# Performance work log

Hardware: AMD Instinct MI355X
Metric: run time of the kernel (lower is better)

The kernel has to match this reference:

```python
import jax, jax.numpy as jnp
import numpy as np

N_NODES = 25000
N_EDGES = 400000
N_GRAPHS = 100
D_IN = 16
D = 32          # node_dim
K = 11          # spectral coefficients = edge_dim
NOUT1 = 30
NOUT2 = 2
L = 2           # n_interactions
D_OUT = 32


def setup_inputs() -> dict:
    key = jax.random.key(0)
    ks = jax.random.split(key, 24)
    s = 0.1
    inp = {
        'x': jax.random.normal(ks[0], (N_NODES, D_IN), jnp.float32),
        'edge_attr': jax.random.uniform(ks[1], (N_EDGES, K), jnp.float32),
        'edge_index': jax.random.randint(ks[2], (2, N_EDGES), 0, N_NODES),
        'batch': jnp.sort(jax.random.randint(ks[3], (N_NODES,), 0, N_GRAPHS)),
        # embedding
        'emb_w': jax.random.normal(ks[4], (D_IN, D)) * s,
        'emb_b': jnp.zeros((D,)),
        # per-interaction params, stacked on leading L axis
        'init_w': jax.random.normal(ks[5], (L, D, D)) * s,             # initial_dense (no bias)
        'e1_w': jax.random.normal(ks[6], (L, K, 2 * K)) * s,
        'e2_w': jax.random.normal(ks[7], (L, K, 2 * K)) * s,
        'e3_w': jax.random.normal(ks[8], (L, K, 2 * K)) * s,
        'e4_w': jax.random.normal(ks[9], (L, 4 * K, K)) * s,
        'conv_w': jax.random.normal(ks[10], (L, K, D, NOUT1)) * s,     # SpectConv weight (selfconn=False)
        'conv_b': jnp.zeros((L, NOUT1)),
        'att_v': jax.random.normal(ks[11], (L, D, 1)) * s,
        'skip1_w': jax.random.normal(ks[12], (L, D, NOUT2)) * s,
        'skip1_b': jnp.full((L, NOUT2), 0.01),
        'skip2_w': jax.random.normal(ks[13], (L, D, NOUT2)) * s,
        'skip2_b': jnp.full((L, NOUT2), 0.01),
        'out_w': jax.random.normal(ks[14], (L, NOUT1 + NOUT2, D)) * s,
        'out_b': jnp.full((L, D), 0.01),
        # encoder output head
        'final_w': jax.random.normal(ks[15], (D, D_OUT)) * s,
        'final_b': jnp.zeros((D_OUT,)),
    }
    return inp


def _segment_softmax(raw, dst, n):
    m = jax.ops.segment_max(raw, dst, num_segments=n)
    m = jnp.where(jnp.isfinite(m), m, 0.0)
    e = jnp.exp(raw - m[dst])
    denom = jax.ops.segment_sum(e, dst, num_segments=n)
    return e / (denom[dst] + 1e-16)


def _interaction(h, src, dst, edge_attr, p):
    (init_w, e1_w, e2_w, e3_w, e4_w, conv_w, conv_b, att_v,
     s1_w, s1_b, s2_w, s2_b, out_w, out_b) = p
    n = h.shape[0]
    h_proj = h @ init_w                                     # [N, D]
    # learned edge transform
    lin = jax.nn.relu(edge_attr @ e1_w)                     # [E, 2K]
    gate = jnp.tanh(edge_attr @ e2_w) * jnp.tanh(edge_attr @ e3_w)
    ea = jax.nn.relu(jnp.concatenate([lin, gate], axis=1) @ e4_w)  # [E, K]
    # spectral conv with attention (selfconn=False)
    xs = h_proj[src]                                        # gather [E, D]
    msgs = ea[:, :, None] * xs[:, None, :]                  # [E, K, D]
    agg = jax.ops.segment_sum(msgs, dst, num_segments=n)    # [N, K, D]
    sum_out = jnp.einsum('nkd,kdo->no', agg, conv_w)        # [N, NOUT1]
    pooled = ea.mean(axis=1, keepdims=True) * xs            # mean_k msg_k, [E, D]
    raw_att = (pooled @ att_v)[:, 0]                        # [E]
    att = _segment_softmax(raw_att, dst, n)                 # [E]
    att_agg = jax.ops.segment_sum(att[:, None, None] * msgs, dst, num_segments=n)
    att_out = jnp.einsum('nkd,kdo->no', att_agg, conv_w)
    conv_out = jax.nn.relu(sum_out + att_out + conv_b)      # [N, NOUT1]
    skip = jnp.tanh(h_proj @ s1_w + s1_b) * jnp.tanh(h_proj @ s2_w + s2_b)  # [N, NOUT2]
    layer_out = jnp.concatenate([conv_out, skip], axis=1)
    delta = layer_out @ out_w + out_b                       # [N, D]
    return delta, att


def reference(x, edge_attr, emb_w, emb_b, init_w, e1_w, e2_w, e3_w, e4_w,
              conv_w, conv_b, att_v, skip1_w, skip1_b, skip2_w, skip2_b,
              out_w, out_b, final_w, final_b, edge_index, batch):
    src, dst = edge_index[0], edge_index[1]
    h = x @ emb_w + emb_b                                   # node embedding [N, D]
    atts = []
    for l in range(L):
        p = (init_w[l], e1_w[l], e2_w[l], e3_w[l], e4_w[l], conv_w[l], conv_b[l],
             att_v[l], skip1_w[l], skip1_b[l], skip2_w[l], skip2_b[l], out_w[l], out_b[l])
        delta, att = _interaction(h, src, dst, edge_attr, p)
        h = h + delta                                       # residual
        atts.append(att)
    # global mean pool per graph
    counts = jax.ops.segment_sum(jnp.ones((h.shape[0],), h.dtype), batch, num_segments=N_GRAPHS)
    pooled = jax.ops.segment_sum(h, batch, num_segments=N_GRAPHS) / jnp.maximum(counts, 1.0)[:, None]
    output = pooled @ final_w + final_b                     # [G, D_OUT]
    return output, h, jnp.stack(atts)
```

## Files before the change

### kernel.cpp

```cpp
#include <hip/hip_runtime.h>
#include <hip/hip_bf16.h>

typedef __hip_bfloat16 bf16;
using f32x4v = __attribute__((ext_vector_type(4))) float;
using bf16x8 = __attribute__((ext_vector_type(8))) short;

#define N_NODES 25000
#define N_PAD   25024
#define N_EDGES 400000
#define N_GR    100

__device__ __forceinline__ bf16 tob(float v) { return __float2bfloat16(v); }
__device__ __forceinline__ unsigned short tobu(float v) {
  union { bf16 b; unsigned short u; } c; c.b = __float2bfloat16(v); return c.u;
}
__device__ __forceinline__ float b2f(unsigned short u) { return __uint_as_float(((unsigned)u) << 16); }
__device__ __forceinline__ float tanh_fast(float x) {
  float cx = fminf(fmaxf(x, -10.f), 10.f);
  float e = __expf(2.f * cx);
  return (e - 1.f) / (e + 1.f);
}

__global__ __launch_bounds__(256) void hist_kernel(const int* __restrict__ dst, int* __restrict__ deg, int E) {
  int e = blockIdx.x * blockDim.x + threadIdx.x;
  if (e < E) atomicAdd(&deg[dst[e]], 1);
}

__global__ __launch_bounds__(1024) void scan_kernel(const int* __restrict__ deg, int* __restrict__ offs,
                                                    int* __restrict__ cur, int n) {
  __shared__ int wsum[16];
  __shared__ int wpre[16];
  int t = threadIdx.x, lane = t & 63, w = t >> 6;
  int carry = 0;
  for (int base = 0; base < n; base += 1024) {
    int v = (base + t < n) ? deg[base + t] : 0;
    int x = v;
    #pragma unroll
    for (int s = 1; s < 64; s <<= 1) { int y = __shfl_up(x, s); if (lane >= s) x += y; }
    if (lane == 63) wsum[w] = x;
    __syncthreads();
    if (w == 0 && lane < 16) {
      int ws_ = wsum[lane];
      int xs = ws_;
      #pragma unroll
      for (int s = 1; s < 16; s <<= 1) { int y = __shfl_up(xs, s); if (lane >= s) xs += y; }
      wpre[lane] = xs - ws_;
    }
    __syncthreads();
    int excl = carry + wpre[w] + x - v;
    if (base + t < n) { offs[base + t] = excl; cur[base + t] = excl; }
    carry += wpre[15] + wsum[15];
    __syncthreads();
  }
  if (t == 0) offs[n] = carry;
}

__global__ __launch_bounds__(256) void fill_kernel(const int* __restrict__ dst, int* __restrict__ cur,
                                                   int* __restrict__ elist, int* __restrict__ epos, int E) {
  int e = blockIdx.x * blockDim.x + threadIdx.x;
  if (e < E) { int p = atomicAdd(&cur[dst[e]], 1); elist[p] = e; epos[e] = p; }
}

__global__ __launch_bounds__(256) void prep_kernel(const float* __restrict__ e1, const float* __restrict__ e2,
                                                   const float* __restrict__ e3, const float* __restrict__ e4,
                                                   const float* __restrict__ attv, const float* __restrict__ convw,
                                                   const float* __restrict__ outw,
                                                   float* __restrict__ wE, bf16* __restrict__ Wt,
                                                   bf16* __restrict__ owB) {
  int i = blockIdx.x * blockDim.x + threadIdx.x;
  if (i < 2 * 1352) {
    int l = i / 1352, r = i % 1352;
    float v = 0.f;
    if (r < 264)       { int q = r;        int j = q / 12, k = q % 12; if (k < 11) v = e1[l*242 + k*22 + j]; }
    else if (r < 528)  { int q = r - 264;  int j = q / 12, k = q % 12; if (k < 11) v = e2[l*242 + k*22 + j]; }
    else if (r < 792)  { int q = r - 528;  int j = q / 12, k = q % 12; if (k < 11) v = e3[l*242 + k*22 + j]; }
    else if (r < 1056) { int q = r - 792;  int j = q / 12, k = q % 12; if (k < 11) v = e4[l*484 + j*11 + k]; }
    else if (r < 1320) { int q = r - 1056; int j = q / 12, k = q % 12; if (k < 11) v = e4[l*484 + (22 + j)*11 + k]; }
    else               { int d = r - 1320; v = attv[l*32 + d]; }
    wE[i] = v;
  }
  int t = i - 2 * 1352;
  if (t >= 0 && t < 2 * 32 * 352) {
    int l = t / (32 * 352), q = t % (32 * 352);
    int o = q / 352, dk = q % 352;
    int d = dk / 11, kk = dk % 11;
    float v = 0.f;
    if (o < 30) v = convw[l*10560 + (kk*32 + d)*30 + o];
    Wt[t] = tob(v);
  }
  int u = i - 2 * 1352 - 2 * 32 * 352;
  if (u >= 0 && u < 2048) {
    int l = u >> 10, rem = u & 1023;
    int hf = rem >> 9, rem2 = rem & 511;
    int lane = rem2 >> 3, j = rem2 & 7;
    int k = (lane >> 4) * 8 + j, n = lane & 15;
    owB[u] = tob(outw[l*1024 + k*32 + hf*16 + n]);
  }
}

__global__ __launch_bounds__(256) void emb_hproj_kernel(const float* __restrict__ x, const float* __restrict__ w,
                                                        const float* __restrict__ b, const float* __restrict__ w1,
                                                        float* __restrict__ h, float* __restrict__ hp,
                                                        unsigned short* __restrict__ hpb, int N) {
  __shared__ float semb[16 * 32];
  __shared__ float sw1[32 * 32];
  __shared__ float sb[32];
  __shared__ float sx[8][16];
  __shared__ float sh[8][33];
  int tid = threadIdx.x;
  for (int i = tid; i < 16 * 32; i += 256) semb[i] = w[i];
  for (int i = tid; i < 32 * 32; i += 256) sw1[i] = w1[i];
  if (tid < 32) sb[tid] = b[tid];
  int nb = blockIdx.x * 8;
  if (tid < 128) {
    int n = nb + (tid >> 4), k = tid & 15;
    sx[tid >> 4][k] = (n < N) ? x[(size_t)n * 16 + k] : 0.f;
  }
  __syncthreads();
  int grp = tid >> 5, d = tid & 31;
  int n = nb + grp;
  float acc = sb[d];
  #pragma unroll
  for (int k = 0; k < 16; k++) acc += sx[grp][k] * semb[k*32 + d];
  sh[grp][d] = acc;
  if (n < N) h[(size_t)n * 32 + d] = acc;
  __syncthreads();
  float hpv = 0.f;
  #pragma unroll
  for (int k = 0; k < 32; k++) hpv += sh[grp][k] * sw1[k*32 + d];
  if (n < N) {
    hp[(size_t)n * 32 + d] = hpv;
    hpb[(size_t)n * 32 + d] = tobu(hpv);
  }
}

__device__ __forceinline__ void loadw12(const float4* base, int idx3, float* w) {
  float4 a = base[idx3], b = base[idx3 + 1], c = base[idx3 + 2];
  w[0]=a.x; w[1]=a.y; w[2]=a.z; w[3]=a.w;
  w[4]=b.x; w[5]=b.y; w[6]=b.z; w[7]=b.w;
  w[8]=c.x; w[9]=c.y; w[10]=c.z; w[11]=c.w;
}

__global__ __launch_bounds__(256) void edge_kernel(const float* __restrict__ eattr,
                                                   const int* __restrict__ srcA,
                                                   const int* __restrict__ epos,
                                                   const unsigned short* __restrict__ hpb,
                                                   const float* __restrict__ wEl,
                                                   uint4* __restrict__ pay, int E) {
  const float4* w4 = (const float4*)wEl;
  int e = blockIdx.x * blockDim.x + threadIdx.x;
  bool live = e < E;
  float a[11], acc[11];
  #pragma unroll
  for (int k = 0; k < 11; k++) {
    a[k] = live ? eattr[(size_t)e*11 + k] : 0.f;
    acc[k] = 0.f;
  }
  for (int j = 0; j < 22; j++) {
    float w[12];
    loadw12(w4, j*3, w);
    float l1 = 0.f;
    #pragma unroll
    for (int k = 0; k < 11; k++) l1 += a[k] * w[k];
    loadw12(w4, 66 + j*3, w);
    float l2 = 0.f;
    #pragma unroll
    for (int k = 0; k < 11; k++) l2 += a[k] * w[k];
    loadw12(w4, 132 + j*3, w);
    float l3 = 0.f;
    #pragma unroll
    for (int k = 0; k < 11; k++) l3 += a[k] * w[k];
    float gg = tanh_fast(l2) * tanh_fast(l3);
    l1 = fmaxf(l1, 0.f);
    float wl[12], wg[12];
    loadw12(w4, 198 + j*3, wl);
    loadw12(w4, 264 + j*3, wg);
    #pragma unroll
    for (int k = 0; k < 11; k++) acc[k] += l1*wl[k] + gg*wg[k];
  }
  if (!live) return;
  const float* av = wEl + 1320;
  float mean = 0.f;
  #pragma unroll
  for (int k = 0; k < 11; k++) { acc[k] = fmaxf(acc[k], 0.f); mean += acc[k]; }
  mean *= (1.f / 11.f);
  int s = srcA[e];
  const uint2* hb = (const uint2*)(hpb + (size_t)s * 32);
  float dot = 0.f;
  #pragma unroll
  for (int q = 0; q < 8; q++) {
    uint2 hv = hb[q];
    dot += b2f((unsigned short)hv.x) * av[q*4+0] + b2f((unsigned short)(hv.x >> 16)) * av[q*4+1]
         + b2f((unsigned short)hv.y) * av[q*4+2] + b2f((unsigned short)(hv.y >> 16)) * av[q*4+3];
  }
  float raw = mean * dot;
  unsigned p[6];
  #pragma unroll
  for (int q = 0; q < 5; q++)
    p[q] = (unsigned)tobu(acc[2*q]) | ((unsigned)tobu(acc[2*q+1]) << 16);
  p[5] = (unsigned)tobu(acc[10]);
  int pp = epos[e];
  pay[(size_t)pp * 2]     = make_uint4(p[0], p[1], p[2], p[3]);
  pay[(size_t)pp * 2 + 1] = make_uint4(p[4], p[5], __float_as_uint(raw), (unsigned)s);
}

__device__ __forceinline__ void unpack_pay(uint4 p0, uint4 p1, float* ev) {
  ev[0] = b2f((unsigned short)p0.x); ev[1] = b2f((unsigned short)(p0.x >> 16));
  ev[2] = b2f((unsigned short)p0.y); ev[3] = b2f((unsigned short)(p0.y >> 16));
  ev[4] = b2f((unsigned short)p0.z); ev[5] = b2f((unsigned short)(p0.z >> 16));
  ev[6] = b2f((unsigned short)p0.w); ev[7] = b2f((unsigned short)(p0.w >> 16));
  ev[8] = b2f((unsigned short)p1.x); ev[9] = b2f((unsigned short)(p1.x >> 16));
  ev[10] = b2f((unsigned short)p1.y);
}

__global__ __launch_bounds__(256) void node_kernel(const int* __restrict__ offs, const int* __restrict__ elist,
                                                   const uint4* __restrict__ pay,
                                                   const unsigned short* __restrict__ hpb,
                                                   bf16* __restrict__ Abuf, float* __restrict__ atts, int N) {
  int wid = threadIdx.x >> 6, lane = threadIdx.x & 63;
  int half = lane >> 5, d = lane & 31;
  int n = blockIdx.x * 4 + wid;
  if (n >= N_PAD) return;
  bool valid = (n < N);
  int beg = 0, deg = 0;
  if (valid) { beg = offs[n]; deg = offs[n + 1] - beg; }

  float agg[11], watt[11];
  #pragma unroll
  for (int k = 0; k < 11; k++) { agg[k] = 0.f; watt[k] = 0.f; }
  float m = -1e30f, denom = 0.f;

  int j = half;
  for (; j + 2 < deg; j += 4) {
    uint4 a0 = pay[(size_t)(beg + j) * 2],     a1 = pay[(size_t)(beg + j) * 2 + 1];
    uint4 b0 = pay[(size_t)(beg + j + 2) * 2], b1 = pay[(size_t)(beg + j + 2) * 2 + 1];
    float xa = b2f(hpb[(size_t)(int)a1.w * 32 + d]);
    float xb = b2f(hpb[(size_t)(int)b1.w * 32 + d]);
    float ra = __uint_as_float(a1.z), rb = __uint_as_float(b1.z);
    float eva[11], evb[11];
    unpack_pay(a0, a1, eva);
    unpack_pay(b0, b1, evb);
    if (ra > m) {
      float sc = __expf(m - ra);
      denom *= sc;
      #pragma unroll
      for (int k = 0; k < 11; k++) watt[k] *= sc;
      m = ra;
    }
    float pa = __expf(ra - m);
    denom += pa;
    #pragma unroll
    for (int k = 0; k < 11; k++) { float t = eva[k]; agg[k] += t * xa; watt[k] += (pa * t) * xa; }
    if (rb > m) {
      float sc = __expf(m - rb);
      denom *= sc;
      #pragma unroll
      for (int k = 0; k < 11; k++) watt[k] *= sc;
      m = rb;
    }
    float pb = __expf(rb - m);
    denom += pb;
    #pragma unroll
    for (int k = 0; k < 11; k++) { float t = evb[k]; agg[k] += t * xb; watt[k] += (pb * t) * xb; }
  }
  for (; j < deg; j += 2) {
    uint4 q0 = pay[(size_t)(beg + j) * 2], q1 = pay[(size_t)(beg + j) * 2 + 1];
    float xs = b2f(hpb[(size_t)(int)q1.w * 32 + d]);
    float r = __uint_as_float(q1.z);
    float ev[11];
    unpack_pay(q0, q1, ev);
    if (r > m) {
      float sc = __expf(m - r);
      denom *= sc;
      #pragma unroll
      for (int k = 0; k < 11; k++) watt[k] *= sc;
      m = r;
    }
    float p = __expf(r - m);
    denom += p;
    #pragma unroll
    for (int k = 0; k < 11; k++) { float t = ev[k]; agg[k] += t * xs; watt[k] += (p * t) * xs; }
  }

  float m_o = __shfl_xor(m, 32);
  float M = fmaxf(m, m_o);
  float ss = __expf(m - M);
  float so = __expf(m_o - M);
  float den_o = __shfl_xor(denom, 32);
  float denT = denom * ss + den_o * so;
  float inv = 1.f / (denT + 1e-16f);
  float comb[11];
  #pragma unroll
  for (int k = 0; k < 11; k++) {
    float ao = __shfl_xor(agg[k], 32);
    float wo = __shfl_xor(watt[k], 32);
    comb[k] = (agg[k] + ao) + (watt[k] * ss + wo * so) * inv;
  }

  if (half == 0) {
    bf16* arow = Abuf + (size_t)n * 352 + d * 11;
    #pragma unroll
    for (int k = 0; k < 11; k++) arow[k] = tob(comb[k]);
  }

  for (int jj = lane; jj < deg; jj += 64) {
    float r = __uint_as_float(pay[(size_t)(beg + jj) * 2 + 1].z);
    atts[elist[beg + jj]] = __expf(r - M) * inv;
  }
}

__global__ __launch_bounds__(256) void convfused_kernel(const short* __restrict__ A, const short* __restrict__ Wt,
                                                        const short* __restrict__ owB,
                                                        const float* __restrict__ hp, float* __restrict__ h,
                                                        const float* __restrict__ convb,
                                                        const float* __restrict__ s1w, const float* __restrict__ s1b,
                                                        const float* __restrict__ s2w, const float* __restrict__ s2b,
                                                        const float* __restrict__ outb,
                                                        const float* __restrict__ initw_next,
                                                        float* __restrict__ hp_out, unsigned short* __restrict__ hpb_out,
                                                        int N) {
  __shared__ short slo[64][40];
  __shared__ float sdelta[64][36];
  __shared__ float sskipw[128];
  __shared__ float sskipb[4];
  __shared__ float scb[32];
  __shared__ float sob[32];
  __shared__ float sw1[1024];
  int tid = threadIdx.x;
  if (tid < 64) sskipw[tid] = s1w[tid];
  if (tid >= 64 && tid < 128) sskipw[tid] = s2w[tid - 64];
  if (tid >= 128 && tid < 160) sob[tid - 128] = outb[tid - 128];
  if (tid >= 160 && tid < 192) scb[tid - 160] = (tid - 160 < 30) ? convb[tid - 160] : 0.f;
  if (tid >= 192 && tid < 196) sskipb[tid - 192] = (tid < 194) ? s1b[tid - 192] : s2b[tid - 194];
  if (initw_next) {
    for (int i = tid; i < 1024; i += 256) sw1[i] = initw_next[i];
  }
  __syncthreads();

  int wave = tid >> 6, lane = tid & 63;
  int r16 = lane & 15, kq = lane >> 4;
  int mbase = blockIdx.x * 64 + wave * 16;

  const short* arow = A + (size_t)(mbase + r16) * 352 + kq * 8;
  const short* b0p = Wt + (size_t)r16 * 352 + kq * 8;
  const short* b1p = b0p + 16 * 352;
  f32x4v acc0 = {0.f, 0.f, 0.f, 0.f}, acc1 = {0.f, 0.f, 0.f, 0.f};
  #pragma unroll
  for (int ks = 0; ks < 11; ks++) {
    bf16x8 af = *(const bf16x8*)(arow + ks * 32);
    bf16x8 b0 = *(const bf16x8*)(b0p + ks * 32);
    bf16x8 b1 = *(const bf16x8*)(b1p + ks * 32);
    acc0 = __builtin_amdgcn_mfma_f32_16x16x32_bf16(af, b0, acc0, 0, 0, 0);
    acc1 = __builtin_amdgcn_mfma_f32_16x16x32_bf16(af, b1, acc1, 0, 0, 0);
  }
  #pragma unroll
  for (int r = 0; r < 4; r++) {
    int row = wave * 16 + kq * 4 + r;
    slo[row][r16] = (short)tobu(fmaxf(acc0[r] + scb[r16], 0.f));
    if (r16 < 14) slo[row][16 + r16] = (short)tobu(fmaxf(acc1[r] + scb[16 + r16], 0.f));
  }
  __syncthreads();

  if (tid < 128) {
    int row = tid >> 1, jx = tid & 1;
    int grow = blockIdx.x * 64 + row;
    float a1 = sskipb[jx], a2 = sskipb[2 + jx];
    if (grow < N) {
      const float* hr = hp + (size_t)grow * 32;
      #pragma unroll
      for (int dd = 0; dd < 32; dd++) {
        float hv = hr[dd];
        a1 += hv * sskipw[dd*2 + jx];
        a2 += hv * sskipw[64 + dd*2 + jx];
      }
    }
    slo[row][30 + jx] = (short)tobu(tanh_fast(a1) * tanh_fast(a2));
  }
  __syncthreads();

  bf16x8 a2f = *(const bf16x8*)&slo[wave * 16 + r16][kq * 8];
  bf16x8 bo0 = *(const bf16x8*)(owB + lane * 8);
  bf16x8 bo1 = *(const bf16x8*)(owB + 512 + lane * 8);
  f32x4v d0 = {0.f, 0.f, 0.f, 0.f}, d1 = {0.f, 0.f, 0.f, 0.f};
  d0 = __builtin_amdgcn_mfma_f32_16x16x32_bf16(a2f, bo0, d0, 0, 0, 0);
  d1 = __builtin_amdgcn_mfma_f32_16x16x32_bf16(a2f, bo1, d1, 0, 0, 0);
  #pragma unroll
  for (int r = 0; r < 4; r++) {
    int row = wave * 16 + kq * 4 + r;
    sdelta[row][r16] = d0[r] + sob[r16];
    sdelta[row][16 + r16] = d1[r] + sob[16 + r16];
  }
  __syncthreads();

  int row = tid >> 2, col0 = (tid & 3) * 8;
  int grow = blockIdx.x * 64 + row;
  if (grow < N) {
    float* hr = h + (size_t)grow * 32 + col0;
    float4 ha = *(float4*)hr;
    float4 hb = *(float4*)(hr + 4);
    float4 da = *(float4*)&sdelta[row][col0];
    float4 db = *(float4*)&sdelta[row][col0 + 4];
    ha.x += da.x; ha.y += da.y; ha.z += da.z; ha.w += da.w;
    hb.x += db.x; hb.y += db.y; hb.z += db.z; hb.w += db.w;
    *(float4*)hr = ha;
    *(float4*)(hr + 4) = hb;
    *(float4*)&sdelta[row][col0] = ha;
    *(float4*)&sdelta[row][col0 + 4] = hb;
  }
  if (initw_next) {
    __syncthreads();
    if (grow < N) {
      float o[8];
      #pragma unroll
      for (int c = 0; c < 8; c++) o[c] = 0.f;
      #pragma unroll
      for (int k = 0; k < 32; k++) {
        float hv = sdelta[row][k];
        #pragma unroll
        for (int c = 0; c < 8; c++) o[c] += hv * sw1[k*32 + col0 + c];
      }
      float* hpo = hp_out + (size_t)grow * 32 + col0;
      unsigned short* hbo = hpb_out + (size_t)grow * 32 + col0;
      #pragma unroll
      for (int c = 0; c < 8; c++) { hpo[c] = o[c]; hbo[c] = tobu(o[c]); }
    }
  }
}

__global__ void bounds_kernel(const int* __restrict__ batch, int* __restrict__ gb) {
  int g = threadIdx.x;
  if (g > N_GR) return;
  if (g == N_GR) { gb[g] = N_NODES; return; }
  int lo = 0, hi = N_NODES;
  while (lo < hi) { int mid = (lo + hi) >> 1; if (batch[mid] < g) lo = mid + 1; else hi = mid; }
  gb[g] = lo;
}

__global__ __launch_bounds__(256) void pool2_kernel(const float* __restrict__ h, const int* __restrict__ gb,
                                                    const float* __restrict__ fw, const float* __restrict__ fb,
                                                    float* __restrict__ out0, float* __restrict__ outh) {
  __shared__ float part[8][32];
  __shared__ float pooled[32];
  int g = blockIdx.x;
  int s = gb[g], e = gb[g + 1];
  int grp = threadIdx.x >> 5, d = threadIdx.x & 31;
  float acc = 0.f;
  for (int n = s + grp; n < e; n += 8) {
    float v = h[(size_t)n * 32 + d];
    outh[(size_t)n * 32 + d] = v;
    acc += v;
  }
  part[grp][d] = acc;
  __syncthreads();
  if (threadIdx.x < 32) {
    float sum = 0.f;
    #pragma unroll
    for (int i = 0; i < 8; i++) sum += part[i][d];
    pooled[d] = sum / fmaxf((float)(e - s), 1.f);
  }
  __syncthreads();
  if (threadIdx.x < 32) {
    int jx = threadIdx.x;
    float o = fb[jx];
    #pragma unroll
    for (int dd = 0; dd < 32; dd++) o += pooled[dd] * fw[dd*32 + jx];
    out0[g * 32 + jx] = o;
  }
}

extern "C" void kernel_launch(void* const* d_in, const int* in_sizes, int n_in,
                              void* d_out, int out_size, void* d_ws, size_t ws_size,
                              hipStream_t stream) {
  (void)in_sizes; (void)n_in; (void)out_size; (void)ws_size;
  const float* x      = (const float*)d_in[0];
  const float* eattr  = (const float*)d_in[1];
  const int* eidx     = (const int*)d_in[2];
  const int* batch    = (const int*)d_in[3];
  const float* emb_w  = (const float*)d_in[4];
  const float* emb_b  = (const float*)d_in[5];
  const float* init_w = (const float*)d_in[6];
  const float* e1w    = (const float*)d_in[7];
  const float* e2w    = (const float*)d_in[8];
  const float* e3w    = (const float*)d_in[9];
  const float* e4w    = (const float*)d_in[10];
  const float* convw  = (const float*)d_in[11];
  const float* convb  = (const float*)d_in[12];
  const float* attv   = (const float*)d_in[13];
  const float* s1w    = (const float*)d_in[14];
  const float* s1b    = (const float*)d_in[15];
  const float* s2w    = (const float*)d_in[16];
  const float* s2b    = (const float*)d_in[17];
  const float* outw   = (const float*)d_in[18];
  const float* outb   = (const float*)d_in[19];
  const float* finw   = (const float*)d_in[20];
  const float* finb   = (const float*)d_in[21];

  char* ws = (char*)d_ws;
  size_t off = 0;
  auto take = [&](size_t bytes) -> char* {
    char* p = ws + off;
    off += (bytes + 255) & ~(size_t)255;
    return p;
  };
  float* h    = (float*)take((size_t)N_NODES * 32 * 4);
  float* hp   = (float*)take((size_t)N_NODES * 32 * 4);
  unsigned short* hpb = (unsigned short*)take((size_t)N_NODES * 32 * 2);
  uint4* pay  = (uint4*)take((size_t)N_EDGES * 32);
  bf16*  Abuf = (bf16*)take((size_t)N_PAD * 352 * 2);
  int*   deg  = (int*)take((size_t)N_NODES * 4);
  int*   offs = (int*)take((size_t)(N_NODES + 1) * 4);
  int*   cur  = (int*)take((size_t)N_NODES * 4);
  int*   elist= (int*)take((size_t)N_EDGES * 4);
  int*   epos = (int*)take((size_t)N_EDGES * 4);
  int*   gb   = (int*)take((size_t)(N_GR + 1) * 4);
  float* wE   = (float*)take((size_t)2 * 1352 * 4);
  bf16*  Wt   = (bf16*)take((size_t)2 * 32 * 352 * 2);
  bf16*  owB  = (bf16*)take((size_t)2048 * 2);

  float* out0 = (float*)d_out;
  float* outh = out0 + N_GR * 32;
  float* outa = outh + (size_t)N_NODES * 32;

  const int* srcA = eidx;
  const int* dstA = eidx + N_EDGES;

  hipMemsetAsync(deg, 0, (size_t)N_NODES * 4, stream);

  prep_kernel<<<107, 256, 0, stream>>>(e1w, e2w, e3w, e4w, attv, convw, outw, wE, Wt, owB);
  hist_kernel<<<(N_EDGES + 255) / 256, 256, 0, stream>>>(dstA, deg, N_EDGES);
  scan_kernel<<<1, 1024, 0, stream>>>(deg, offs, cur, N_NODES);
  fill_kernel<<<(N_EDGES + 255) / 256, 256, 0, stream>>>(dstA, cur, elist, epos, N_EDGES);
  emb_hproj_kernel<<<(N_NODES + 7) / 8, 256, 0, stream>>>(x, emb_w, emb_b, init_w, h, hp, hpb, N_NODES);
  bounds_kernel<<<1, 128, 0, stream>>>(batch, gb);

  for (int l = 0; l < 2; l++) {
    edge_kernel<<<(N_EDGES + 255) / 256, 256, 0, stream>>>(
        eattr, srcA, epos, hpb, wE + l * 1352, pay, N_EDGES);
    node_kernel<<<N_PAD / 4, 256, 0, stream>>>(offs, elist, pay, hpb,
                                               Abuf, outa + (size_t)l * N_EDGES, N_NODES);
    convfused_kernel<<<N_PAD / 64, 256, 0, stream>>>(
        (const short*)Abuf, (const short*)Wt + (size_t)l * 32 * 352, (const short*)owB + (size_t)l * 1024,
        hp, h, convb + l * 30, s1w + l * 64, s1b + l * 2, s2w + l * 64, s2b + l * 2,
        outb + l * 32,
        (l == 0) ? (init_w + 1024) : nullptr, hp, hpb, N_NODES);
  }

  pool2_kernel<<<N_GR, 256, 0, stream>>>(h, gb, finw, finb, out0, outh);
}
```

Baseline: 257.8 us.

## Precompute per-node softmax stats and fold attention weight into aggregation coefficient

The node kernel's online-softmax aggregation is replaced by two short wave-wide passes that find each node's max and denominator, then writes attention values. The main edge loop then accumulates with a single scalar coefficient (1 + attention) per edge, so the separate watt accumulators, rescaling branches and cross-half merge go away. The bounds computation moves into prep_kernel to save a launch, and tanh_fast drops its clamp and uses a hardware reciprocal. In exchange, each edge's payload score is read two more times, and tanh now relies on exp overflow behaving well.

```diff
diff --git a/kernel.cpp b/kernel.cpp
--- a/kernel.cpp
+++ b/kernel.cpp
@@ -16,9 +16,8 @@
 }
 __device__ __forceinline__ float b2f(unsigned short u) { return __uint_as_float(((unsigned)u) << 16); }
 __device__ __forceinline__ float tanh_fast(float x) {
-  float cx = fminf(fmaxf(x, -10.f), 10.f);
-  float e = __expf(2.f * cx);
-  return (e - 1.f) / (e + 1.f);
+  float e = __expf(2.f * x);
+  return 1.f - 2.f * __builtin_amdgcn_rcpf(e + 1.f);
 }
 
 __global__ __launch_bounds__(256) void hist_kernel(const int* __restrict__ dst, int* __restrict__ deg, int E) {
@@ -65,8 +64,9 @@
                                                    const float* __restrict__ e3, const float* __restrict__ e4,
                                                    const float* __restrict__ attv, const float* __restrict__ convw,
                                                    const float* __restrict__ outw,
+                                                   const int* __restrict__ batch,
                                                    float* __restrict__ wE, bf16* __restrict__ Wt,
-                                                   bf16* __restrict__ owB) {
+                                                   bf16* __restrict__ owB, int* __restrict__ gb) {
   int i = blockIdx.x * blockDim.x + threadIdx.x;
   if (i < 2 * 1352) {
     int l = i / 1352, r = i % 1352;
@@ -95,6 +95,15 @@
     int lane = rem2 >> 3, j = rem2 & 7;
     int k = (lane >> 4) * 8 + j, n = lane & 15;
     owB[u] = tob(outw[l*1024 + k*32 + hf*16 + n]);
+  }
+  int g = i - 2 * 1352 - 2 * 32 * 352 - 2048;
+  if (g >= 0 && g <= N_GR) {
+    if (g == N_GR) { gb[g] = N_NODES; }
+    else {
+      int lo = 0, hi = N_NODES;
+      while (lo < hi) { int mid = (lo + hi) >> 1; if (batch[mid] < g) lo = mid + 1; else hi = mid; }
+      gb[g] = lo;
+    }
   }
 }
 
@@ -221,14 +230,32 @@
   int half = lane >> 5, d = lane & 31;
   int n = blockIdx.x * 4 + wid;
   if (n >= N_PAD) return;
-  bool valid = (n < N);
   int beg = 0, deg = 0;
-  if (valid) { beg = offs[n]; deg = offs[n + 1] - beg; }
-
-  float agg[11], watt[11];
-  #pragma unroll
-  for (int k = 0; k < 11; k++) { agg[k] = 0.f; watt[k] = 0.f; }
-  float m = -1e30f, denom = 0.f;
+  if (n < N) { beg = offs[n]; deg = offs[n + 1] - beg; }
+  const float* payf = (const float*)pay;
+
+  float m_l = -1e30f;
+  for (int jj = lane; jj < deg; jj += 64)
+    m_l = fmaxf(m_l, payf[(size_t)(beg + jj) * 8 + 6]);
+  #pragma unroll
+  for (int s = 1; s < 64; s <<= 1) m_l = fmaxf(m_l, __shfl_xor(m_l, s));
+  float M = m_l;
+
+  float s_l = 0.f;
+  for (int jj = lane; jj < deg; jj += 64)
+    s_l += __expf(payf[(size_t)(beg + jj) * 8 + 6] - M);
+  #pragma unroll
+  for (int s = 1; s < 64; s <<= 1) s_l += __shfl_xor(s_l, s);
+  float inv = 1.f / (s_l + 1e-16f);
+
+  for (int jj = lane; jj < deg; jj += 64) {
+    float r = payf[(size_t)(beg + jj) * 8 + 6];
+    atts[elist[beg + jj]] = __expf(r - M) * inv;
+  }
+
+  float agg[11];
+  #pragma unroll
+  for (int k = 0; k < 11; k++) agg[k] = 0.f;
 
   int j = half;
   for (; j + 2 < deg; j += 4) {
@@ -236,76 +263,33 @@
     uint4 b0 = pay[(size_t)(beg + j + 2) * 2], b1 = pay[(size_t)(beg + j + 2) * 2 + 1];
     float xa = b2f(hpb[(size_t)(int)a1.w * 32 + d]);
     float xb = b2f(hpb[(size_t)(int)b1.w * 32 + d]);
-    float ra = __uint_as_float(a1.z), rb = __uint_as_float(b1.z);
+    float ca = 1.f + __expf(__uint_as_float(a1.z) - M) * inv;
+    float cb = 1.f + __expf(__uint_as_float(b1.z) - M) * inv;
+    float cxa = ca * xa, cxb = cb * xb;
     float eva[11], evb[11];
     unpack_pay(a0, a1, eva);
     unpack_pay(b0, b1, evb);
-    if (ra > m) {
-      float sc = __expf(m - ra);
-      denom *= sc;
-      #pragma unroll
-      for (int k = 0; k < 11; k++) watt[k] *= sc;
-      m = ra;
-    }
-    float pa = __expf(ra - m);
-    denom += pa;
-    #pragma unroll
-    for (int k = 0; k < 11; k++) { float t = eva[k]; agg[k] += t * xa; watt[k] += (pa * t) * xa; }
-    if (rb > m) {
-      float sc = __expf(m - rb);
-      denom *= sc;
-      #pragma unroll
-      for (int k = 0; k < 11; k++) watt[k] *= sc;
-      m = rb;
-    }
-    float pb = __expf(rb - m);
-    denom += pb;
-    #pragma unroll
-    for (int k = 0; k < 11; k++) { float t = evb[k]; agg[k] += t * xb; watt[k] += (pb * t) * xb; }
+    #pragma unroll
+    for (int k = 0; k < 11; k++) agg[k] += eva[k] * cxa + evb[k] * cxb;
   }
   for (; j < deg; j += 2) {
     uint4 q0 = pay[(size_t)(beg + j) * 2], q1 = pay[(size_t)(beg + j) * 2 + 1];
     float xs = b2f(hpb[(size_t)(int)q1.w * 32 + d]);
-    float r = __uint_as_float(q1.z);
+    float c = 1.f + __expf(__uint_as_float(q1.z) - M) * inv;
+    float cx = c * xs;
     float ev[11];
     unpack_pay(q0, q1, ev);
-    if (r > m) {
-      float sc = __expf(m - r);
-      denom *= sc;
-      #pragma unroll
-      for (int k = 0; k < 11; k++) watt[k] *= sc;
-      m = r;
-    }
-    float p = __expf(r - m);
-    denom += p;
-    #pragma unroll
-    for (int k = 0; k < 11; k++) { float t = ev[k]; agg[k] += t * xs; watt[k] += (p * t) * xs; }
-  }
-
-  float m_o = __shfl_xor(m, 32);
-  float M = fmaxf(m, m_o);
-  float ss = __expf(m - M);
-  float so = __expf(m_o - M);
-  float den_o = __shfl_xor(denom, 32);
-  float denT = denom * ss + den_o * so;
-  float inv = 1.f / (denT + 1e-16f);
-  float comb[11];
-  #pragma unroll
-  for (int k = 0; k < 11; k++) {
-    float ao = __shfl_xor(agg[k], 32);
-    float wo = __shfl_xor(watt[k], 32);
-    comb[k] = (agg[k] + ao) + (watt[k] * ss + wo * so) * inv;
-  }
+    #pragma unroll
+    for (int k = 0; k < 11; k++) agg[k] += ev[k] * cx;
+  }
+
+  #pragma unroll
+  for (int k = 0; k < 11; k++) agg[k] += __shfl_xor(agg[k], 32);
 
   if (half == 0) {
     bf16* arow = Abuf + (size_t)n * 352 + d * 11;
     #pragma unroll
-    for (int k = 0; k < 11; k++) arow[k] = tob(comb[k]);
-  }
-
-  for (int jj = lane; jj < deg; jj += 64) {
-    float r = __uint_as_float(pay[(size_t)(beg + jj) * 2 + 1].z);
-    atts[elist[beg + jj]] = __expf(r - M) * inv;
+    for (int k = 0; k < 11; k++) arow[k] = tob(agg[k]);
   }
 }
 
@@ -425,15 +409,6 @@
       for (int c = 0; c < 8; c++) { hpo[c] = o[c]; hbo[c] = tobu(o[c]); }
     }
   }
-}
-
-__global__ void bounds_kernel(const int* __restrict__ batch, int* __restrict__ gb) {
-  int g = threadIdx.x;
-  if (g > N_GR) return;
-  if (g == N_GR) { gb[g] = N_NODES; return; }
-  int lo = 0, hi = N_NODES;
-  while (lo < hi) { int mid = (lo + hi) >> 1; if (batch[mid] < g) lo = mid + 1; else hi = mid; }
-  gb[g] = lo;
 }
 
 __global__ __launch_bounds__(256) void pool2_kernel(const float* __restrict__ h, const int* __restrict__ gb,
@@ -526,12 +501,11 @@
 
   hipMemsetAsync(deg, 0, (size_t)N_NODES * 4, stream);
 
-  prep_kernel<<<107, 256, 0, stream>>>(e1w, e2w, e3w, e4w, attv, convw, outw, wE, Wt, owB);
+  prep_kernel<<<107, 256, 0, stream>>>(e1w, e2w, e3w, e4w, attv, convw, outw, batch, wE, Wt, owB, gb);
   hist_kernel<<<(N_EDGES + 255) / 256, 256, 0, stream>>>(dstA, deg, N_EDGES);
   scan_kernel<<<1, 1024, 0, stream>>>(deg, offs, cur, N_NODES);
   fill_kernel<<<(N_EDGES + 255) / 256, 256, 0, stream>>>(dstA, cur, elist, epos, N_EDGES);
   emb_hproj_kernel<<<(N_NODES + 7) / 8, 256, 0, stream>>>(x, emb_w, emb_b, init_w, h, hp, hpb, N_NODES);
-  bounds_kernel<<<1, 128, 0, stream>>>(batch, gb);
 
   for (int l = 0; l < 2; l++) {
     edge_kernel<<<(N_EDGES + 255) / 256, 256, 0, stream>>>(
```

Measured after the change: 246.5 us. -4.4%, faster.
